# Kernel tuning notes

Hardware: AMD Instinct MI355X
Metric: run time of the kernel (lower is better)

## Reference

```python
import jax, jax.numpy as jnp
import numpy as np

B, S, D = 4, 2048, 1024  # batch, seq_len, input_dimension
KD, VD = 1024, 1024      # key_dim, value_dim


def setup_inputs() -> dict:
    key = jax.random.key(0)
    ks = jax.random.split(key, 9)
    sc_in = 1.0 / np.sqrt(D)
    sc_v = 1.0 / np.sqrt(VD)
    return {
        "x":  jax.random.normal(ks[0], (B, S, D), dtype=jnp.float32),
        "Wq": jax.random.normal(ks[1], (KD, D), dtype=jnp.float32) * sc_in,
        "bq": jax.random.normal(ks[2], (KD,), dtype=jnp.float32) * 0.01,
        "Wk": jax.random.normal(ks[3], (KD, D), dtype=jnp.float32) * sc_in,
        "bk": jax.random.normal(ks[4], (KD,), dtype=jnp.float32) * 0.01,
        "Wv": jax.random.normal(ks[5], (VD, D), dtype=jnp.float32) * sc_in,
        "bv": jax.random.normal(ks[6], (VD,), dtype=jnp.float32) * 0.01,
        "Wo": jax.random.normal(ks[7], (D, VD), dtype=jnp.float32) * sc_v,
        "bo": jax.random.normal(ks[8], (D,), dtype=jnp.float32) * 0.01,
    }


def reference(x, Wq, bq, Wk, bk, Wv, bv, Wo, bo):
    # projections (torch Linear: x @ W.T + b)
    q = jnp.einsum('bsd,kd->bsk', x, Wq) + bq   # (B,S,KD)
    k = jnp.einsum('bsd,kd->bsk', x, Wk) + bk   # (B,S,KD)
    v = jnp.einsum('bsd,vd->bsv', x, Wv) + bv   # (B,S,VD)

    scores = jnp.einsum('bqk,bsk->bqs', q, k) / jnp.sqrt(jnp.float32(KD))  # (B,S,S)

    # sign rescale: scores * sign(scores) (sign(0) mapped to 1) == |scores| with zeros kept
    sign_mask = jnp.sign(scores)
    sign_mask = sign_mask + (sign_mask == 0).astype(jnp.float32)

    # causal mask: lower-triangular (incl diag) multiplied by 1, strict upper -> -inf
    seq = scores.shape[-1]
    causal = jnp.tril(jnp.ones((seq, seq), dtype=bool))
    masked = jnp.where(causal, scores * sign_mask, -jnp.inf)

    weights = jax.nn.softmax(masked, axis=2)            # (B,S,S)
    out = jnp.einsum('bqs,bsv->bqv', weights, v)        # (B,S,VD)
    return jnp.einsum('bqv,dv->bqd', out, Wo) + bo      # (B,S,D)
```

## Files before the change

### kernel.cpp

```cpp
#include <hip/hip_runtime.h>
#include <hip/hip_bf16.h>
#include <cstdint>


typedef __attribute__((ext_vector_type(8))) __bf16 bf16x8;
typedef __attribute__((ext_vector_type(4))) __bf16 bf16x4;
typedef __attribute__((ext_vector_type(4))) float floatx4;

struct Ptr3 { const float* p[3]; };

__device__ __forceinline__ void async_copy16(const __bf16* g, const __bf16* l) {
  __builtin_amdgcn_global_load_lds(
      (const __attribute__((address_space(1))) unsigned int*)(const void*)g,
      (__attribute__((address_space(3))) unsigned int*)(unsigned)(uintptr_t)(const void*)l,
      16, 0, 0);
}

__device__ __forceinline__ void gemm_core8p(const __bf16* __restrict__ pA,
                                            const __bf16* __restrict__ pB,
                                            int K, int nT, int mb, int nb,
                                            floatx4 (&acc)[8][4]) {
  __shared__ __align__(16) __bf16 As[2][16384];
  __shared__ __align__(16) __bf16 Bs[2][16384];

  const int t = threadIdx.x;
  const int lane = t & 63;
  const int wave = t >> 6;
  const int quad = lane >> 4;
  const int l16 = lane & 15;
  const int wm = wave >> 2;
  const int wn = wave & 3;

  const int r0 = t >> 3;
  const int csw = ((t & 7) ^ (r0 & 7)) * 8;
  const __bf16* gA = pA + (long)(mb * 256 + r0) * K + csw;
  const __bf16* gB = pB + (long)(nb * 256 + r0) * K + csw;
  const long row64 = (long)64 * K;
  const long row128 = (long)128 * K;

  auto stageA = [&](int kt, int half) {
    const long ko = (long)kt * 64 + (long)half * row128;
    __bf16* d = &As[kt & 1][half * 8192 + t * 8];
    async_copy16(gA + ko, d);
    async_copy16(gA + ko + row64, d + 4096);
  };
  auto stageB = [&](int kt, int half) {
    const long ko = (long)kt * 64 + (long)half * row128;
    __bf16* d = &Bs[kt & 1][half * 8192 + t * 8];
    async_copy16(gB + ko, d);
    async_copy16(gB + ko + row64, d + 4096);
  };
  auto cl = [&](int kt) { return kt < nT ? kt : nT - 1; };

  bf16x8 af[4][2], bfr[2][2];
  auto ldsA = [&](int buf, int ihalf) {
#pragma unroll
    for (int i2 = 0; i2 < 4; ++i2) {
      const int rl = wm * 64 + i2 * 16 + l16;
      const int rb = ihalf * 8192 + rl * 64;
      const int key = rl & 7;
#pragma unroll
      for (int ks = 0; ks < 2; ++ks)
        af[i2][ks] = *(const bf16x8*)&As[buf][rb + (((ks * 4 + quad) ^ key) << 3)];
    }
  };
  auto ldsB = [&](int buf, int jhalf) {
#pragma unroll
    for (int j2 = 0; j2 < 2; ++j2) {
      const int rl = wn * 32 + j2 * 16 + l16;
      const int rb = jhalf * 8192 + rl * 64;
      const int key = rl & 7;
#pragma unroll
      for (int ks = 0; ks < 2; ++ks)
        bfr[j2][ks] = *(const bf16x8*)&Bs[buf][rb + (((ks * 4 + quad) ^ key) << 3)];
    }
  };
  auto mfmaQ = [&](int ihalf, int jhalf) {
    __builtin_amdgcn_s_setprio(1);
#pragma unroll
    for (int ks = 0; ks < 2; ++ks)
#pragma unroll
      for (int i2 = 0; i2 < 4; ++i2)
#pragma unroll
        for (int j2 = 0; j2 < 2; ++j2)
          acc[ihalf * 4 + i2][jhalf * 2 + j2] =
              __builtin_amdgcn_mfma_f32_16x16x32_bf16(
                  af[i2][ks], bfr[j2][ks],
                  acc[ihalf * 4 + i2][jhalf * 2 + j2], 0, 0, 0);
    __builtin_amdgcn_s_setprio(0);
  };

#define VM6 asm volatile("s_waitcnt vmcnt(6)" ::: "memory")
#define PHASE(LDSOP, STAGEOP, WAITOP, IH, JH)                 \
  LDSOP;                                                      \
  STAGEOP;                                                    \
  WAITOP;                                                     \
  __builtin_amdgcn_sched_barrier(0);                          \
  __builtin_amdgcn_s_barrier();                               \
  asm volatile("s_waitcnt lgkmcnt(0)" ::: "memory");          \
  __builtin_amdgcn_sched_barrier(0);                          \
  mfmaQ(IH, JH);                                              \
  __builtin_amdgcn_s_barrier();

  stageA(0, 0); stageB(0, 0); stageB(0, 1); stageA(0, 1);
  stageA(1, 0); stageB(1, 1); stageA(1, 1);
  VM6;
  __builtin_amdgcn_s_barrier();
  __builtin_amdgcn_sched_barrier(0);

  const int nIter = nT >> 1;
  for (int it = 0, T = 0; it < nIter; ++it, T += 2) {
    PHASE((ldsA(0, 0), ldsB(0, 0)), stageB(cl(T + 1), 0), (void)0, 0, 0)
    PHASE(ldsB(0, 1),               stageA(cl(T + 2), 0), (void)0, 0, 1)
    PHASE(ldsA(0, 1),               stageB(cl(T + 2), 1), (void)0, 1, 1)
    PHASE(ldsB(0, 0),               stageA(cl(T + 2), 1), VM6,     1, 0)
    PHASE((ldsA(1, 0), ldsB(1, 0)), stageB(cl(T + 2), 0), (void)0, 0, 0)
    PHASE(ldsB(1, 1),               stageA(cl(T + 3), 0), (void)0, 0, 1)
    PHASE(ldsA(1, 1),               stageB(cl(T + 3), 1), (void)0, 1, 1)
    PHASE(ldsB(1, 0),               stageA(cl(T + 3), 1), VM6,     1, 0)
  }
  __syncthreads();
#undef PHASE
#undef VM6
}


__global__ void prep2b(const float* __restrict__ Wo, Ptr3 tp,
                       const float* __restrict__ bv, const float* __restrict__ bq,
                       const float* __restrict__ bk, const float* __restrict__ x,
                       __bf16* __restrict__ Wob, __bf16* __restrict__ Wqt,
                       __bf16* __restrict__ Wkt, __bf16* __restrict__ Wvt,
                       __bf16* __restrict__ xb, float* __restrict__ bvo,
                       float* __restrict__ cscal, float* __restrict__ lsum) {
  __shared__ __bf16 tile[64][66];
  __shared__ float wsum[4];
  const int bid = blockIdx.x;
  const int t = threadIdx.x;
  if (bid >= 2818) {
    const long i = ((long)(bid - 2818) * 256 + t) * 4;
    const float4 f = *(const float4*)(x + i);
    bf16x4 o;
    o[0] = (__bf16)f.x; o[1] = (__bf16)f.y; o[2] = (__bf16)f.z; o[3] = (__bf16)f.w;
    *(bf16x4*)(xb + i) = o;
  } else if (bid < 1024) {
    const long e = ((long)bid * 256 + t) * 4;
    const float4 f = *(const float4*)(Wo + e);
    bf16x4 o;
    o[0] = (__bf16)f.x; o[1] = (__bf16)f.y; o[2] = (__bf16)f.z; o[3] = (__bf16)f.w;
    *(bf16x4*)(Wob + e) = o;
  } else if (bid < 1792) {
    const int seg = (bid - 1024) >> 8;
    const int idx = (bid - 1024) & 255;
    const float* src = tp.p[seg];
    __bf16* dstw = seg == 0 ? Wqt : (seg == 1 ? Wkt : Wvt);
    const int r0 = (idx >> 4) * 64, c0 = (idx & 15) * 64;
#pragma unroll
    for (int e = 0; e < 16; ++e) {
      const int i = e * 256 + t;
      const int r = i >> 6, c = i & 63;
      tile[r][c] = (__bf16)src[(long)(r0 + r) * 1024 + (c0 + c)];
    }
    __syncthreads();
#pragma unroll
    for (int e = 0; e < 16; ++e) {
      const int i = e * 256 + t;
      const int r = i >> 6, c = i & 63;
      dstw[(long)(c0 + r) * 1024 + (r0 + c)] = tile[c][r];
    }
  } else if (bid < 2816) {
    const int d = bid - 1792;
    const float* row = Wo + (long)d * 1024;
    float s = 0.f;
    for (int v = t; v < 1024; v += 256) s += bv[v] * row[v];
#pragma unroll
    for (int off = 32; off > 0; off >>= 1) s += __shfl_down(s, off, 64);
    if ((t & 63) == 0) wsum[t >> 6] = s;
    __syncthreads();
    if (t == 0) bvo[d] = wsum[0] + wsum[1] + wsum[2] + wsum[3];
  } else if (bid == 2816) {
    float s = 0.f;
    for (int i = t; i < 1024; i += 256) s += bq[i] * bk[i];
#pragma unroll
    for (int off = 32; off > 0; off >>= 1) s += __shfl_down(s, off, 64);
    if ((t & 63) == 0) wsum[t >> 6] = s;
    __syncthreads();
    if (t == 0) *cscal = wsum[0] + wsum[1] + wsum[2] + wsum[3];
  } else {
#pragma unroll
    for (int e = 0; e < 8; ++e)
      *(float4*)(lsum + (e * 256 + t) * 4) = float4{0.f, 0.f, 0.f, 0.f};
  }
}

__global__ void __launch_bounds__(512, 2)
gemmW(const __bf16* __restrict__ Wkt, const __bf16* __restrict__ Wqt,
      const __bf16* __restrict__ Wob, const __bf16* __restrict__ Wvt,
      __bf16* __restrict__ Mt, __bf16* __restrict__ Wvo,
      const float* __restrict__ bk, const float* __restrict__ bq,
      float* __restrict__ m1f, float* __restrict__ m2f) {
  const int id = blockIdx.x;
  const int t = threadIdx.x;

  if (id >= 32) {
    const int g = id - 32;
    const bool isM2 = g >= 16;
    const int q = g & 15;
    const __bf16* Wt = isM2 ? Wkt : Wqt;
    const float* bvec = isM2 ? bq : bk;
    float* dst = isM2 ? m2f : m1f;
    const int row = q * 64 + (t >> 3);
    const int l8 = t & 7;
    const __bf16* wr = Wt + (long)row * 1024 + l8 * 128;
    const float* bp = bvec + l8 * 128;
    float s = 0.f;
#pragma unroll
    for (int jj = 0; jj < 16; ++jj) {
      bf16x8 wv = *(const bf16x8*)(wr + jj * 8);
#pragma unroll
      for (int e = 0; e < 8; ++e) s += (float)wv[e] * bp[jj * 8 + e];
    }
    s += __shfl_xor(s, 1, 64);
    s += __shfl_xor(s, 2, 64);
    s += __shfl_xor(s, 4, 64);
    if (l8 == 0) dst[row] = s;
    return;
  }

  const bool isMt = id < 16;
  const int w = isMt ? id : id - 16;
  const int mb = w >> 2, nb = w & 3;
  const __bf16* pA = isMt ? Wkt : Wob;
  const __bf16* pB = isMt ? Wqt : Wvt;
  __bf16* dst = isMt ? Mt : Wvo;

  floatx4 acc[8][4] = {};
  gemm_core8p(pA, pB, 1024, 16, mb, nb, acc);

  const int lane = t & 63, wave = t >> 6;
  const int quad = lane >> 4, l16 = lane & 15;
  const int wm = wave >> 2, wn = wave & 3;
#pragma unroll
  for (int j = 0; j < 4; ++j) {
    const int gc = nb * 256 + (j >> 1) * 128 + wn * 32 + (j & 1) * 16 + l16;
#pragma unroll
    for (int i = 0; i < 8; ++i) {
      const int gr = mb * 256 + (i >> 2) * 128 + wm * 64 + (i & 3) * 16 + quad * 4;
#pragma unroll
      for (int r = 0; r < 4; ++r)
        dst[(long)(gr + r) * 1024 + gc] = (__bf16)acc[i][j][r];
    }
  }
}

__global__ void __launch_bounds__(512, 2)
big1(const __bf16* __restrict__ xb, const __bf16* __restrict__ Mt,
     const __bf16* __restrict__ Wvo, const float* __restrict__ m2f,
     const float* __restrict__ bvo, __bf16* __restrict__ y2,
     __bf16* __restrict__ Ut, const float* __restrict__ m1f,
     const float* __restrict__ cscal, float* __restrict__ uvec,
     int S, int D) {
  const int id = blockIdx.x;
  const int t = threadIdx.x;

  if (id >= 256) {
    const int k = id - 256;
    const int row = k * 64 + (t >> 3);
    const int l8 = t & 7;
    const float c = *cscal;
    const __bf16* xr = xb + (long)row * 1024 + l8 * 128;
    const float* mp = m1f + l8 * 128;
    float s = 0.f;
#pragma unroll
    for (int jj = 0; jj < 16; ++jj) {
      bf16x8 xv = *(const bf16x8*)(xr + jj * 8);
#pragma unroll
      for (int e = 0; e < 8; ++e) s += (float)xv[e] * mp[jj * 8 + e];
    }
    s += __shfl_xor(s, 1, 64);
    s += __shfl_xor(s, 2, 64);
    s += __shfl_xor(s, 4, 64);
    if (l8 == 0) uvec[row] = s + c;
    return;
  }

  const bool isY2 = id < 128;
  const int w = isY2 ? id : id - 128;
  const int mb = w >> 2;
  const int nb = w & 3;
  const __bf16* pB = isY2 ? Mt : Wvo;

  floatx4 acc[8][4] = {};
  gemm_core8p(xb, pB, 1024, 16, mb, nb, acc);

  const int lane = t & 63, wave = t >> 6;
  const int quad = lane >> 4, l16 = lane & 15;
  const int wm = wave >> 2, wn = wave & 3;

  if (isY2) {
#pragma unroll
    for (int j = 0; j < 4; ++j) {
      const int gc = nb * 256 + (j >> 1) * 128 + wn * 32 + (j & 1) * 16 + l16;
      const float bvv = m2f[gc];
#pragma unroll
      for (int i = 0; i < 8; ++i) {
        const int gr = mb * 256 + (i >> 2) * 128 + wm * 64 + (i & 3) * 16 + quad * 4;
#pragma unroll
        for (int r = 0; r < 4; ++r)
          y2[(long)(gr + r) * 1024 + gc] = (__bf16)(acc[i][j][r] + bvv);
      }
    }
  } else {
    const int bb = (mb * 256) / S;
    const int s0 = mb * 256 - bb * S;
#pragma unroll
    for (int j = 0; j < 4; ++j) {
      const int gc = nb * 256 + (j >> 1) * 128 + wn * 32 + (j & 1) * 16 + l16;
      const float bv = bvo[gc];
#pragma unroll
      for (int i = 0; i < 8; ++i) {
        const int sr = s0 + (i >> 2) * 128 + wm * 64 + (i & 3) * 16 + quad * 4;
        bf16x4 o;
#pragma unroll
        for (int r = 0; r < 4; ++r) o[r] = (__bf16)(acc[i][j][r] + bv);
        *(bf16x4*)&Ut[((long)bb * D + gc) * S + sr] = o;
      }
    }
  }
}

__global__ void __launch_bounds__(512, 2)
scoresP(const __bf16* __restrict__ xb, const __bf16* __restrict__ y2,
        const float* __restrict__ uvec, __bf16* __restrict__ P,
        float* __restrict__ lsum, int S, int KD) {
  const int id = blockIdx.x;
  const int b = id / 36;
  const int r = id - b * 36;
  int mb = 0;
  while ((mb + 1) * (mb + 2) / 2 <= r) ++mb;
  const int nb = r - mb * (mb + 1) / 2;

  floatx4 acc[8][4] = {};
  gemm_core8p(y2 + (long)b * S * KD, xb + (long)b * S * KD, KD, 16, mb, nb, acc);

  const int t = threadIdx.x;
  const int lane = t & 63, wave = t >> 6;
  const int quad = lane >> 4, l16 = lane & 15;
  const int wm = wave >> 2, wn = wave & 3;

  __bf16* C = P + (long)b * S * S;
  float* lrow = lsum + (long)b * S;
  const float sc = 0.03125f;
#pragma unroll
  for (int i = 0; i < 8; ++i) {
#pragma unroll
    for (int r4 = 0; r4 < 4; ++r4) {
      const int row = mb * 256 + (i >> 2) * 128 + wm * 64 + (i & 3) * 16 + quad * 4 + r4;
      const float urow = uvec[(long)b * S + row];
      float psum = 0.f;
#pragma unroll
      for (int j = 0; j < 4; ++j) {
        const int col = nb * 256 + (j >> 1) * 128 + wn * 32 + (j & 1) * 16 + l16;
        const float p =
            (col <= row) ? __expf(fabsf(acc[i][j][r4] + urow) * sc) : 0.f;
        psum += p;
        C[(long)row * S + col] = (__bf16)p;
      }
      psum += __shfl_xor(psum, 1, 64);
      psum += __shfl_xor(psum, 2, 64);
      psum += __shfl_xor(psum, 4, 64);
      psum += __shfl_xor(psum, 8, 64);
      if (l16 == 0) atomicAdd(&lrow[row], psum);
    }
  }
}

__global__ void __launch_bounds__(512, 2)
gemm_pvo(const __bf16* __restrict__ P, const __bf16* __restrict__ Ut,
         const float* __restrict__ lsum, const float* __restrict__ bo,
         float* __restrict__ out, int S, int D) {
  const int id = blockIdx.x;
  const int b = id >> 5;
  const int idx = id & 31;
  const int mb = idx >> 2;
  const int nb = idx & 3;

  floatx4 acc[8][4] = {};
  gemm_core8p(P + (long)b * S * S, Ut + (long)b * D * S, S, 4 * (mb + 1), mb,
              nb, acc);

  const int t = threadIdx.x;
  const int lane = t & 63, wave = t >> 6;
  const int quad = lane >> 4, l16 = lane & 15;
  const int wm = wave >> 2, wn = wave & 3;
  const float* lrow = lsum + (long)b * S;

#pragma unroll
  for (int i = 0; i < 8; ++i) {
#pragma unroll
    for (int r = 0; r < 4; ++r) {
      const int row = mb * 256 + (i >> 2) * 128 + wm * 64 + (i & 3) * 16 + quad * 4 + r;
      const float inv = 1.f / lrow[row];
#pragma unroll
      for (int j = 0; j < 4; ++j) {
        const int col = nb * 256 + (j >> 1) * 128 + wn * 32 + (j & 1) * 16 + l16;
        out[((long)b * S + row) * D + col] = acc[i][j][r] * inv + bo[col];
      }
    }
  }
}

extern "C" void kernel_launch(void* const* d_in, const int* in_sizes, int n_in,
                              void* d_out, int out_size, void* d_ws, size_t ws_size,
                              hipStream_t stream) {
  const float* x = (const float*)d_in[0];
  const float* Wq = (const float*)d_in[1];
  const float* bq = (const float*)d_in[2];
  const float* Wk = (const float*)d_in[3];
  const float* bk = (const float*)d_in[4];
  const float* Wv = (const float*)d_in[5];
  const float* bv = (const float*)d_in[6];
  const float* Wo = (const float*)d_in[7];
  const float* bo = (const float*)d_in[8];
  float* out = (float*)d_out;

  constexpr int B = 4, S = 2048, D = 1024, KD = 1024;
  constexpr long MB_ = 1024 * 1024;

  char* w = (char*)d_ws;
  __bf16* xb  = (__bf16*)(w);
  __bf16* y2  = (__bf16*)(w + 16 * MB_);
  __bf16* Ut  = (__bf16*)(w + 32 * MB_);
  __bf16* P   = (__bf16*)(w + 48 * MB_);
  __bf16* Wob = (__bf16*)(w + 80 * MB_);
  __bf16* Wqt = (__bf16*)(w + 82 * MB_);
  __bf16* Wkt = (__bf16*)(w + 84 * MB_);
  __bf16* Wvt = (__bf16*)(w + 86 * MB_);
  __bf16* Mt  = (__bf16*)(w + 88 * MB_);
  __bf16* Wvo = (__bf16*)(w + 90 * MB_);
  float* lsum  = (float*)(w + 92 * MB_);
  float* uvec  = (float*)(w + 92 * MB_ + 32768);
  float* bvo   = (float*)(w + 92 * MB_ + 65536);
  float* m2f   = (float*)(w + 92 * MB_ + 69632);
  float* m1f   = (float*)(w + 92 * MB_ + 73728);
  float* cscal = (float*)(w + 92 * MB_ + 77824);

  Ptr3 tp{{Wq, Wk, Wv}};
  prep2b<<<11010, 256, 0, stream>>>(Wo, tp, bv, bq, bk, x, Wob, Wqt, Wkt,
                                    Wvt, xb, bvo, cscal, lsum);

  gemmW<<<64, 512, 0, stream>>>(Wkt, Wqt, Wob, Wvt, Mt, Wvo, bk, bq, m1f, m2f);

  big1<<<384, 512, 0, stream>>>(xb, Mt, Wvo, m2f, bvo, y2, Ut, m1f, cscal,
                                uvec, S, D);

  scoresP<<<144, 512, 0, stream>>>(xb, y2, uvec, P, lsum, S, KD);

  gemm_pvo<<<128, 512, 0, stream>>>(P, Ut, lsum, bo, out, S, D);
}
```

Measured before the change: 269.1 us.

## Split-K the heavy causal rows of the PV·Wo GEMM and fold x conversion into gemmW

The P·Ut GEMM has causal row-blocks whose K length grows with the row index. The four heaviest row-blocks per batch are now split into two K-halves, which caps per-block work near the light blocks and spreads 192 blocks over the CUs. The heavy halves write fp32 partials into a reused workspace region, and a new combine kernel sums them, normalizes by the row sums and adds the bias. The x-to-bf16 conversion also moves from the prep kernel into the small 64-block weight GEMM launch so it can fill idle CUs there. The trade-off is an extra launch plus partial-sum traffic in exchange for better load balance on the critical GEMM.

```diff
diff --git a/kernel.cpp b/kernel.cpp
--- a/kernel.cpp
+++ b/kernel.cpp
@@ -125,24 +125,18 @@
 }
 
 
-__global__ void prep2b(const float* __restrict__ Wo, Ptr3 tp,
-                       const float* __restrict__ bv, const float* __restrict__ bq,
-                       const float* __restrict__ bk, const float* __restrict__ x,
-                       __bf16* __restrict__ Wob, __bf16* __restrict__ Wqt,
-                       __bf16* __restrict__ Wkt, __bf16* __restrict__ Wvt,
-                       __bf16* __restrict__ xb, float* __restrict__ bvo,
-                       float* __restrict__ cscal, float* __restrict__ lsum) {
+__global__ void prepW(const float* __restrict__ Wo, Ptr3 tp,
+                      const float* __restrict__ bv, const float* __restrict__ bq,
+                      const float* __restrict__ bk,
+                      __bf16* __restrict__ Wob, __bf16* __restrict__ Wqt,
+                      __bf16* __restrict__ Wkt, __bf16* __restrict__ Wvt,
+                      float* __restrict__ bvo, float* __restrict__ cscal,
+                      float* __restrict__ lsum) {
   __shared__ __bf16 tile[64][66];
   __shared__ float wsum[4];
   const int bid = blockIdx.x;
   const int t = threadIdx.x;
-  if (bid >= 2818) {
-    const long i = ((long)(bid - 2818) * 256 + t) * 4;
-    const float4 f = *(const float4*)(x + i);
-    bf16x4 o;
-    o[0] = (__bf16)f.x; o[1] = (__bf16)f.y; o[2] = (__bf16)f.z; o[3] = (__bf16)f.w;
-    *(bf16x4*)(xb + i) = o;
-  } else if (bid < 1024) {
+  if (bid < 1024) {
     const long e = ((long)bid * 256 + t) * 4;
     const float4 f = *(const float4*)(Wo + e);
     bf16x4 o;
@@ -193,14 +187,23 @@
 }
 
 __global__ void __launch_bounds__(512, 2)
-gemmW(const __bf16* __restrict__ Wkt, const __bf16* __restrict__ Wqt,
-      const __bf16* __restrict__ Wob, const __bf16* __restrict__ Wvt,
-      __bf16* __restrict__ Mt, __bf16* __restrict__ Wvo,
-      const float* __restrict__ bk, const float* __restrict__ bq,
-      float* __restrict__ m1f, float* __restrict__ m2f) {
+gemmWX(const __bf16* __restrict__ Wkt, const __bf16* __restrict__ Wqt,
+       const __bf16* __restrict__ Wob, const __bf16* __restrict__ Wvt,
+       __bf16* __restrict__ Mt, __bf16* __restrict__ Wvo,
+       const float* __restrict__ bk, const float* __restrict__ bq,
+       float* __restrict__ m1f, float* __restrict__ m2f,
+       const float* __restrict__ x, __bf16* __restrict__ xb) {
   const int id = blockIdx.x;
   const int t = threadIdx.x;
 
+  if (id >= 64) {
+    const long i = ((long)(id - 64) * 512 + t) * 4;
+    const float4 f = *(const float4*)(x + i);
+    bf16x4 o;
+    o[0] = (__bf16)f.x; o[1] = (__bf16)f.y; o[2] = (__bf16)f.z; o[3] = (__bf16)f.w;
+    *(bf16x4*)(xb + i) = o;
+    return;
+  }
   if (id >= 32) {
     const int g = id - 32;
     const bool isM2 = g >= 16;
@@ -375,38 +378,99 @@
 }
 
 __global__ void __launch_bounds__(512, 2)
-gemm_pvo(const __bf16* __restrict__ P, const __bf16* __restrict__ Ut,
-         const float* __restrict__ lsum, const float* __restrict__ bo,
-         float* __restrict__ out, int S, int D) {
+pvoS(const __bf16* __restrict__ P, const __bf16* __restrict__ Ut,
+     const float* __restrict__ lsum, const float* __restrict__ bo,
+     float* __restrict__ out, float* __restrict__ part, int S, int D) {
   const int id = blockIdx.x;
-  const int b = id >> 5;
-  const int idx = id & 31;
-  const int mb = idx >> 2;
-  const int nb = idx & 3;
+  const int t = threadIdx.x;
+
+  const __bf16 *pA, *pB;
+  int nT, mb, nb, b, khalf = 0;
+  bool heavy;
+  if (id < 128) {
+    heavy = true;
+    khalf = id & 1;
+    const int rest = id >> 1;
+    nb = rest & 3;
+    const int mbh = (rest >> 2) & 3;
+    b = rest >> 4;
+    mb = 4 + mbh;
+    nT = 2 * (mb + 1);
+    const long koff = (long)khalf * nT * 64;
+    pA = P + (long)b * S * S + koff;
+    pB = Ut + (long)b * D * S + koff;
+  } else {
+    heavy = false;
+    const int l = id - 128;
+    nb = l & 3;
+    mb = (l >> 2) & 3;
+    b = l >> 4;
+    nT = 4 * (mb + 1);
+    pA = P + (long)b * S * S;
+    pB = Ut + (long)b * D * S;
+  }
 
   floatx4 acc[8][4] = {};
-  gemm_core8p(P + (long)b * S * S, Ut + (long)b * D * S, S, 4 * (mb + 1), mb,
-              nb, acc);
-
-  const int t = threadIdx.x;
+  gemm_core8p(pA, pB, S, nT, mb, nb, acc);
+
   const int lane = t & 63, wave = t >> 6;
   const int quad = lane >> 4, l16 = lane & 15;
   const int wm = wave >> 2, wn = wave & 3;
-  const float* lrow = lsum + (long)b * S;
-
-#pragma unroll
-  for (int i = 0; i < 8; ++i) {
-#pragma unroll
-    for (int r = 0; r < 4; ++r) {
-      const int row = mb * 256 + (i >> 2) * 128 + wm * 64 + (i & 3) * 16 + quad * 4 + r;
-      const float inv = 1.f / lrow[row];
-#pragma unroll
-      for (int j = 0; j < 4; ++j) {
-        const int col = nb * 256 + (j >> 1) * 128 + wn * 32 + (j & 1) * 16 + l16;
-        out[((long)b * S + row) * D + col] = acc[i][j][r] * inv + bo[col];
+
+  if (heavy) {
+    float* ps = part + ((long)((b * 4 + (mb - 4)) * 2 + khalf)) * 256 * 1024;
+#pragma unroll
+    for (int i = 0; i < 8; ++i) {
+#pragma unroll
+      for (int r = 0; r < 4; ++r) {
+        const int lr = (i >> 2) * 128 + wm * 64 + (i & 3) * 16 + quad * 4 + r;
+#pragma unroll
+        for (int j = 0; j < 4; ++j) {
+          const int col = nb * 256 + (j >> 1) * 128 + wn * 32 + (j & 1) * 16 + l16;
+          ps[(long)lr * 1024 + col] = acc[i][j][r];
+        }
       }
     }
-  }
+  } else {
+    const float* lrow = lsum + (long)b * S;
+#pragma unroll
+    for (int i = 0; i < 8; ++i) {
+#pragma unroll
+      for (int r = 0; r < 4; ++r) {
+        const int row = mb * 256 + (i >> 2) * 128 + wm * 64 + (i & 3) * 16 + quad * 4 + r;
+        const float inv = 1.f / lrow[row];
+#pragma unroll
+        for (int j = 0; j < 4; ++j) {
+          const int col = nb * 256 + (j >> 1) * 128 + wn * 32 + (j & 1) * 16 + l16;
+          out[((long)b * S + row) * D + col] = acc[i][j][r] * inv + bo[col];
+        }
+      }
+    }
+  }
+}
+
+__global__ void combineH(const float* __restrict__ part,
+                         const float* __restrict__ lsum,
+                         const float* __restrict__ bo, float* __restrict__ out,
+                         int S, int D) {
+  const int hr = blockIdx.x;
+  const int t = threadIdx.x;
+  const int b = hr >> 10;
+  const int lr = hr & 1023;
+  const int mbh = lr >> 8;
+  const int r256 = lr & 255;
+  const int srow = (4 + mbh) * 256 + r256;
+  const float inv = 1.f / lsum[(long)b * S + srow];
+  const long base = (long)((b * 4 + mbh) * 2) * 256 * 1024 + (long)r256 * 1024;
+  const float4 p0 = *(const float4*)(part + base + t * 4);
+  const float4 p1 = *(const float4*)(part + base + 256 * 1024 + t * 4);
+  const float4 bv = *(const float4*)(bo + t * 4);
+  float4 o;
+  o.x = (p0.x + p1.x) * inv + bv.x;
+  o.y = (p0.y + p1.y) * inv + bv.y;
+  o.z = (p0.z + p1.z) * inv + bv.z;
+  o.w = (p0.w + p1.w) * inv + bv.w;
+  *(float4*)(out + ((long)b * S + srow) * D + t * 4) = o;
 }
 
 extern "C" void kernel_launch(void* const* d_in, const int* in_sizes, int n_in,
@@ -443,17 +507,21 @@
   float* m2f   = (float*)(w + 92 * MB_ + 69632);
   float* m1f   = (float*)(w + 92 * MB_ + 73728);
   float* cscal = (float*)(w + 92 * MB_ + 77824);
+  float* part  = (float*)(w);
 
   Ptr3 tp{{Wq, Wk, Wv}};
-  prep2b<<<11010, 256, 0, stream>>>(Wo, tp, bv, bq, bk, x, Wob, Wqt, Wkt,
-                                    Wvt, xb, bvo, cscal, lsum);
-
-  gemmW<<<64, 512, 0, stream>>>(Wkt, Wqt, Wob, Wvt, Mt, Wvo, bk, bq, m1f, m2f);
+  prepW<<<2818, 256, 0, stream>>>(Wo, tp, bv, bq, bk, Wob, Wqt, Wkt, Wvt,
+                                  bvo, cscal, lsum);
+
+  gemmWX<<<4160, 512, 0, stream>>>(Wkt, Wqt, Wob, Wvt, Mt, Wvo, bk, bq,
+                                   m1f, m2f, x, xb);
 
   big1<<<384, 512, 0, stream>>>(xb, Mt, Wvo, m2f, bvo, y2, Ut, m1f, cscal,
                                 uvec, S, D);
 
   scoresP<<<144, 512, 0, stream>>>(xb, y2, uvec, P, lsum, S, KD);
 
-  gemm_pvo<<<128, 512, 0, stream>>>(P, Ut, lsum, bo, out, S, D);
-}
+  pvoS<<<192, 512, 0, stream>>>(P, Ut, lsum, bo, out, part, S, D);
+
+  combineH<<<4096, 256, 0, stream>>>(part, lsum, bo, out, S, D);
+}
```

Result: faster. 253.3 us (-5.9%).
